# Kernel tuning notes

Hardware: AMD Instinct MI355X
Metric: run time of the kernel (lower is better)

Reference implementation:

```python
import jax, jax.numpy as jnp
import numpy as np

B, K, N, NBR = 4, 2048, 8192, 32
DIM, C_IN, W_HID, C_MID, F_HID, C_OUT = 3, 16, 32, 16, 64, 64
BIG = 3000.0


def _mlp(x, w1, b1, w2, b2):
    # SetTransform with one hidden layer, reduction='none': Linear->ReLU->Linear
    return jnp.maximum(x @ w1 + b1, 0.0) @ w2 + b2


def setup_inputs() -> dict:
    key = jax.random.key(0)
    ks = jax.random.split(key, 12)
    s = lambda fan_in: 1.0 / np.sqrt(fan_in)
    return {
        "keys": jax.random.normal(ks[0], (B, K, DIM), jnp.float32),
        "points": jax.random.normal(ks[1], (B, N, DIM), jnp.float32),
        "feats": jax.random.normal(ks[2], (B, N, C_IN), jnp.float32),
        "valid": jax.random.bernoulli(ks[3], 0.95, (B, K, N)),
        "ww1": jax.random.normal(ks[4], (DIM, W_HID), jnp.float32) * s(DIM),
        "wb1": jax.random.normal(ks[5], (W_HID,), jnp.float32) * s(DIM),
        "ww2": jax.random.normal(ks[6], (W_HID, C_MID), jnp.float32) * s(W_HID),
        "wb2": jax.random.normal(ks[7], (C_MID,), jnp.float32) * s(W_HID),
        "fw1": jax.random.normal(ks[8], (C_IN * C_MID, F_HID), jnp.float32) * s(C_IN * C_MID),
        "fb1": jax.random.normal(ks[9], (F_HID,), jnp.float32) * s(C_IN * C_MID),
        "fw2": jax.random.normal(ks[10], (F_HID, C_OUT), jnp.float32) * s(F_HID),
        "fb2": jax.random.normal(ks[11], (C_OUT,), jnp.float32) * s(F_HID),
    }


def reference(keys, points, feats, valid, ww1, wb1, ww2, wb2, fw1, fb1, fw2, fb2):
    # --- dist_fn (Euclidean): dist_vec = points - keys, dist = ||dist_vec|| ---
    diff = points[:, None, :, :] - keys[:, :, None, :]        # [B,K,N,DIM]
    dist = jnp.sqrt(jnp.sum(diff * diff, axis=-1))            # [B,K,N]
    big_dist = dist.max() * BIG
    dist = dist + jnp.where(valid, 0.0, big_dist)
    # --- kNN: smallest NBR distances per key ---
    _, idxs = jax.lax.top_k(-dist, NBR)                       # [B,K,NBR]
    bidx = jnp.arange(B)[:, None, None]
    # gather neighbor info (avoids materializing [B,K,N,*] gathered copies)
    n_rel = points[bidx, idxs] - keys[:, :, None, :]          # [B,K,NBR,DIM]
    n_feats = feats[bidx, idxs]                               # [B,K,NBR,C_IN]
    n_valid = jnp.take_along_axis(valid, idxs, axis=2)        # [B,K,NBR]
    n_valid = n_valid[..., None].astype(n_rel.dtype)
    # per-neighbor weight MLP, mask, batched matmul reduce over neighbors
    m = _mlp(n_rel, ww1, wb1, ww2, wb2) * n_valid             # [B,K,NBR,C_MID]
    nf = n_feats * n_valid                                    # [B,K,NBR,C_IN]
    e = jnp.einsum('bkqm,bkqc->bkmc', m, nf)                  # [B,K,C_MID,C_IN]
    e = e.reshape(B, K, C_MID * C_IN)
    return _mlp(e, fw1, fb1, fw2, fb2)                        # [B,K,C_OUT]
```

## Files before the change

kernel.cpp:

```cpp
#include <hip/hip_runtime.h>
#include <hip/hip_bf16.h>
#include <cstdint>
#include <cstddef>

#define B_    4
#define K_    2048
#define N_    8192
#define NBR_  32
#define NCAND 44
#define SELCAP 64
#define CIN   16
#define WHID  32
#define CMID  16
#define FHID  64
#define COUT  64
#define SOA_OFF 4096
#define WS_NEED ((size_t)SOA_OFF + (size_t)B_ * 3 * N_ * 4 + 4096 )

__global__ void pc_detect_kernel(const unsigned* __restrict__ v, int* __restrict__ flag) {
    const unsigned w = v[threadIdx.x & 63];
    const int byte_like = (((w & 0xFEFEFEFEu) == 0u) && ((w & 0xFFFFFF00u) != 0u)) ? 1 : 0;
    const unsigned long long m = __ballot(byte_like);
    if (threadIdx.x == 0) *flag = (m != 0ull) ? 1 : 0;
}

__global__ __launch_bounds__(256) void pc_soa_kernel(const float* __restrict__ pts,
                                                     float* __restrict__ soa) {
    const int i = blockIdx.x * 256 + threadIdx.x;
    const int b = i >> 13, n = i & (N_ - 1);
    const int t = n >> 8, w = n & 255;
    const float* p = pts + (size_t)i * 3;
    const float x = p[0], y = p[1], z = p[2];
    float* d = soa + (size_t)b * 3 * N_ + (size_t)t * 768 + w;
    d[0]   = x;
    d[256] = y;
    d[512] = z;
}

__device__ __forceinline__ unsigned umin_(unsigned a, unsigned b) { return a < b ? a : b; }

__device__ __forceinline__ unsigned med3_(unsigned a, unsigned b, unsigned c) {
    unsigned d;
    asm("v_med3_u32 %0, %1, %2, %3" : "=v"(d) : "v"(a), "v"(b), "v"(c));
    return d;
}
__device__ __forceinline__ void insert_m3(unsigned (&sa)[8], unsigned kv) {
#pragma unroll
    for (int i = 7; i >= 1; --i)
        sa[i] = med3_(sa[i - 1], sa[i], kv);
    sa[0] = umin_(sa[0], kv);
}

__device__ __forceinline__ void scan_tiled(const float* __restrict__ soa_b,
                                           float kx, float ky, float kz,
                                           int lane, unsigned (&sa)[8]) {
    const int voff = lane * 4;
    const float* p  = soa_b;
    float4 X = *(const float4*)(p + voff);
    float4 Y = *(const float4*)(p + 256 + voff);
    float4 Z = *(const float4*)(p + 512 + voff);
    unsigned vn = (unsigned)voff;
#pragma unroll 2
    for (int t = 0; t < 32; ++t) {
        const float4 cX = X, cY = Y, cZ = Z;
        const float* pn = p + 768;
        X = *(const float4*)(pn + voff);
        Y = *(const float4*)(pn + 256 + voff);
        Z = *(const float4*)(pn + 512 + voff);
        p = pn;
        float dx, dy, dz, d2;
#define PC_ONE(J, XX, YY, ZZ)                                                      \
        dx = XX - kx; dy = YY - ky; dz = ZZ - kz;                                  \
        d2 = fmaf(dz, dz, fmaf(dy, dy, dx * dx));                                  \
        insert_m3(sa, (__float_as_uint(d2) & 0xFFFFE000u) | (vn | J##u));
        PC_ONE(0, cX.x, cY.x, cZ.x)
        PC_ONE(1, cX.y, cY.y, cZ.y)
        PC_ONE(2, cX.z, cY.z, cZ.z)
        PC_ONE(3, cX.w, cY.w, cZ.w)
#undef PC_ONE
        vn += 256u;
    }
}

__device__ __forceinline__ void scan_aos4(const float* __restrict__ pts,
                                          float kx, float ky, float kz,
                                          int lane, unsigned (&sa)[8]) {
    const int l4 = lane * 4;
#pragma unroll 2
    for (int t = 0; t < N_ / 256; ++t) {
        const int n0 = t * 256 + l4;
        const float4* p4 = (const float4*)(pts + (size_t)n0 * 3);
        const float4 A = p4[0], Bv = p4[1], Cv = p4[2];
        float dx, dy, dz, d2;
        dx = A.x - kx; dy = A.y - ky; dz = A.z - kz;
        d2 = fmaf(dz, dz, fmaf(dy, dy, dx * dx));
        insert_m3(sa, (__float_as_uint(d2) & 0xFFFFE000u) | (unsigned)(n0 + 0));
        dx = A.w - kx; dy = Bv.x - ky; dz = Bv.y - kz;
        d2 = fmaf(dz, dz, fmaf(dy, dy, dx * dx));
        insert_m3(sa, (__float_as_uint(d2) & 0xFFFFE000u) | (unsigned)(n0 + 1));
        dx = Bv.z - kx; dy = Bv.w - ky; dz = Cv.x - kz;
        d2 = fmaf(dz, dz, fmaf(dy, dy, dx * dx));
        insert_m3(sa, (__float_as_uint(d2) & 0xFFFFE000u) | (unsigned)(n0 + 2));
        dx = Cv.y - kx; dy = Cv.z - ky; dz = Cv.w - kz;
        d2 = fmaf(dz, dz, fmaf(dy, dy, dx * dx));
        insert_m3(sa, (__float_as_uint(d2) & 0xFFFFE000u) | (unsigned)(n0 + 3));
    }
}

struct SelBuf {
    unsigned cnt;
    unsigned pad;
    unsigned key[SELCAP];
    unsigned long long fk[SELCAP];
};
struct Slice {
    union {
        SelBuf   sel;
        float    w[NBR_ * CMID];
        float    pad_[512];
    } A;
    union {
        float nf[NBR_ * CIN];
        struct { float hp[4 * FHID]; float hf[FHID]; } h;
    } Bv;
    union {
        unsigned slot[NBR_];
        float    e[CMID * CIN];
    } C;
};

template <int SOA>
__global__ __launch_bounds__(128, 8) void pc_main_kernel(
    const float* __restrict__ keys,
    const float* __restrict__ points,
    const float* __restrict__ soa,
    const float* __restrict__ feats,
    const void*  __restrict__ validp,
    const float* __restrict__ ww1, const float* __restrict__ wb1,
    const float* __restrict__ ww2, const float* __restrict__ wb2,
    const float* __restrict__ fw1, const float* __restrict__ fb1,
    const float* __restrict__ fw2, const float* __restrict__ fb2,
    float* __restrict__ out,
    const int* __restrict__ flagp)
{
    __shared__ Slice sl[2];

    const int lane = threadIdx.x & 63;
    const int wv   = threadIdx.x >> 6;
    const int row  = (blockIdx.x << 1) | wv;
    const int b    = row >> 11;
    Slice& S = sl[wv];

    const float kx = keys[row * 3 + 0];
    const float ky = keys[row * 3 + 1];
    const float kz = keys[row * 3 + 2];
    const float* pts = points + (size_t)b * N_ * 3;

    unsigned sa[8];
#pragma unroll
    for (int i = 0; i < 8; ++i) sa[i] = 0xFFFFFFFFu;

    if (SOA) scan_tiled(soa + (size_t)b * 3 * N_, kx, ky, kz, lane, sa);
    else     scan_aos4(pts, kx, ky, kz, lane, sa);

    unsigned hi[8];
#pragma unroll
    for (int s = 0; s < 8; ++s) hi[s] = sa[s] >> 13;

    unsigned want = 0u;
    int need = NCAND;
    for (int bb = 18; bb >= 0; --bb) {
        want <<= 1;
        int cnt0 = 0;
#pragma unroll
        for (int s = 0; s < 8; ++s)
            cnt0 += (int)__popcll(__ballot((hi[s] >> bb) == want));
        if (cnt0 < need) { need -= cnt0; want |= 1u; }
    }

    if (lane == 0) S.A.sel.cnt = 0u;
    int c = 0;
#pragma unroll
    for (int s = 0; s < 8; ++s) c += (hi[s] <= want) ? 1 : 0;
    unsigned base = 0u;
    if (c > 0) base = atomicAdd(&S.A.sel.cnt, (unsigned)c);
#pragma unroll
    for (int s = 0; s < 8; ++s)
        if (s < c && base + (unsigned)s < (unsigned)SELCAP)
            S.A.sel.key[base + s] = sa[s];
    unsigned stot = S.A.sel.cnt;
    stot = (unsigned)__builtin_amdgcn_readfirstlane((int)stot);
    if (stot > (unsigned)SELCAP) stot = SELCAP;
    asm volatile("" ::: "memory");

    if (lane < NBR_) S.C.slot[lane] = 0xFFFFFFFFu;

    const unsigned selkey = S.A.sel.key[(unsigned)lane < stot ? lane : 0];
    const int cidx = (int)(selkey & 8191u);
    unsigned vbit = 0u;
    unsigned long long fkey = ~0ull;
    if ((unsigned)lane < stot) {
        const float cdx = pts[cidx * 3 + 0] - kx;
        const float cdy = pts[cidx * 3 + 1] - ky;
        const float cdz = pts[cidx * 3 + 2] - kz;
        const float cd2 = fmaf(cdz, cdz, fmaf(cdy, cdy, cdx * cdx));
        const int flag = *flagp;
        const size_t vbase = (size_t)row * N_;
        if (flag) vbit = ((const unsigned char*)validp)[vbase + (size_t)cidx];
        else      vbit = ((const unsigned*)validp)[vbase + (size_t)cidx];
        const unsigned d2bits = (vbit != 0u) ? __float_as_uint(cd2) : 0xFFFFFFFFu;
        fkey = ((unsigned long long)d2bits << 13) | (unsigned long long)cidx;
        S.A.sel.fk[lane] = fkey;
    }
    asm volatile("" ::: "memory");

    {
        int rank = 0;
#pragma unroll 4
        for (unsigned j = 0; j < stot; ++j) {
            const unsigned long long fj = S.A.sel.fk[j];
            rank += (fj < fkey) ? 1 : 0;
        }
        if ((unsigned)lane < stot && vbit != 0u && rank < NBR_)
            S.C.slot[rank] = selkey;
    }
    asm volatile("" ::: "memory");

    const int q    = lane & 31;
    const int half = lane >> 5;
    const unsigned skey = S.C.slot[q];
    const int   nidx = (int)(skey & 8191u);
    const float vf   = (skey < 0xF0000000u) ? 1.0f : 0.0f;

    const float rx = pts[nidx * 3 + 0] - kx;
    const float ry = pts[nidx * 3 + 1] - ky;
    const float rz = pts[nidx * 3 + 2] - kz;
    asm volatile("" ::: "memory");

    float wacc[8];
    {
        const float4 b0 = *(const float4*)&wb2[half * 8 + 0];
        const float4 b1 = *(const float4*)&wb2[half * 8 + 4];
        wacc[0] = b0.x; wacc[1] = b0.y; wacc[2] = b0.z; wacc[3] = b0.w;
        wacc[4] = b1.x; wacc[5] = b1.y; wacc[6] = b1.z; wacc[7] = b1.w;
    }

#pragma unroll 8
    for (int j = 0; j < WHID; ++j) {
        float hj = fmaf(rx, ww1[j], fmaf(ry, ww1[WHID + j], fmaf(rz, ww1[2 * WHID + j], wb1[j])));
        hj = fmaxf(hj, 0.0f);
        const float4 wa = *(const float4*)&ww2[j * CMID + half * 8 + 0];
        const float4 wb = *(const float4*)&ww2[j * CMID + half * 8 + 4];
        wacc[0] = fmaf(hj, wa.x, wacc[0]);
        wacc[1] = fmaf(hj, wa.y, wacc[1]);
        wacc[2] = fmaf(hj, wa.z, wacc[2]);
        wacc[3] = fmaf(hj, wa.w, wacc[3]);
        wacc[4] = fmaf(hj, wb.x, wacc[4]);
        wacc[5] = fmaf(hj, wb.y, wacc[5]);
        wacc[6] = fmaf(hj, wb.z, wacc[6]);
        wacc[7] = fmaf(hj, wb.w, wacc[7]);
    }
#pragma unroll
    for (int m = 0; m < 8; ++m) wacc[m] *= vf;

    *(float4*)&S.A.w[q * CMID + half * 8 + 0] = make_float4(wacc[0], wacc[1], wacc[2], wacc[3]);
    *(float4*)&S.A.w[q * CMID + half * 8 + 4] = make_float4(wacc[4], wacc[5], wacc[6], wacc[7]);

    const float* fp = feats + ((size_t)b * N_ + (size_t)nidx) * CIN + half * 8;
    *(float4*)&S.Bv.nf[q * CIN + half * 8 + 0] = *(const float4*)(fp + 0);
    *(float4*)&S.Bv.nf[q * CIN + half * 8 + 4] = *(const float4*)(fp + 4);
    asm volatile("" ::: "memory");

    {
        const int m  = lane >> 2;
        const int c4 = lane & 3;
        float4 eacc = make_float4(0.f, 0.f, 0.f, 0.f);
#pragma unroll
        for (int qq = 0; qq < NBR_; ++qq) {
            const float  wq = S.A.w[qq * CMID + m];
            const float4 f  = *(const float4*)&S.Bv.nf[qq * CIN + c4 * 4];
            eacc.x = fmaf(wq, f.x, eacc.x);
            eacc.y = fmaf(wq, f.y, eacc.y);
            eacc.z = fmaf(wq, f.z, eacc.z);
            eacc.w = fmaf(wq, f.w, eacc.w);
        }
        *(float4*)&S.C.e[m * CIN + c4 * 4] = eacc;
    }
    asm volatile("" ::: "memory");

    {
        const int g  = lane >> 4;
        const int t4 = lane & 15;
        float a0 = 0.f, a1 = 0.f, a2 = 0.f, a3 = 0.f;
#pragma unroll 8
        for (int i = 0; i < 64; ++i) {
            const float  ev = S.C.e[g * 64 + i];
            const float4 wv2 = *(const float4*)&fw1[(size_t)(g * 64 + i) * FHID + t4 * 4];
            a0 = fmaf(ev, wv2.x, a0);
            a1 = fmaf(ev, wv2.y, a1);
            a2 = fmaf(ev, wv2.z, a2);
            a3 = fmaf(ev, wv2.w, a3);
        }
        *(float4*)&S.Bv.h.hp[g * FHID + t4 * 4] = make_float4(a0, a1, a2, a3);
    }
    asm volatile("" ::: "memory");

    {
        float hf = fb1[lane] + S.Bv.h.hp[lane] + S.Bv.h.hp[FHID + lane]
                 + S.Bv.h.hp[2 * FHID + lane] + S.Bv.h.hp[3 * FHID + lane];
        S.Bv.h.hf[lane] = fmaxf(hf, 0.0f);
    }
    asm volatile("" ::: "memory");

    {
        float oacc = fb2[lane];
#pragma unroll 8
        for (int j = 0; j < FHID; ++j)
            oacc = fmaf(S.Bv.h.hf[j], fw2[(size_t)j * COUT + lane], oacc);
        out[(size_t)row * COUT + lane] = oacc;
    }
}

extern "C" void kernel_launch(void* const* d_in, const int* in_sizes, int n_in,
                              void* d_out, int out_size, void* d_ws, size_t ws_size,
                              hipStream_t stream) {
    const float* keys   = (const float*)d_in[0];
    const float* points = (const float*)d_in[1];
    const float* feats  = (const float*)d_in[2];
    const void*  valid  = d_in[3];
    const float* ww1 = (const float*)d_in[4];
    const float* wb1 = (const float*)d_in[5];
    const float* ww2 = (const float*)d_in[6];
    const float* wb2 = (const float*)d_in[7];
    const float* fw1 = (const float*)d_in[8];
    const float* fb1 = (const float*)d_in[9];
    const float* fw2 = (const float*)d_in[10];
    const float* fb2 = (const float*)d_in[11];
    float* out = (float*)d_out;
    int*   flag = (int*)d_ws;
    float* soa  = (float*)((char*)d_ws + SOA_OFF);

    pc_detect_kernel<<<1, 64, 0, stream>>>((const unsigned*)valid, flag);

    if (ws_size >= WS_NEED) {
        pc_soa_kernel<<<(B_ * N_) / 256, 256, 0, stream>>>(points, soa);
        pc_main_kernel<1><<<(B_ * K_) / 2, 128, 0, stream>>>(
            keys, points, soa, feats, valid,
            ww1, wb1, ww2, wb2, fw1, fb1, fw2, fb2, out, flag);
    } else {
        pc_main_kernel<0><<<(B_ * K_) / 2, 128, 0, stream>>>(
            keys, points, soa, feats, valid,
            ww1, wb1, ww2, wb2, fw1, fb1, fw2, fb2, out, flag);
    }
}
```

Before: 394.9 us.

## Stage point tiles in shared memory shared across four waves per block

Blocks grow from two to four waves (one key row each), and the SoA point coordinates are cooperatively loaded into a double-buffered LDS tile, so the four waves share each global load instead of each wave streaming the whole point set from memory. A __syncthreads per tile adds barrier cost across 32 tiles, and LDS use rises with four slices per block, which can lower occupancy. The Slice storage is unioned with the staging buffer.

```diff
diff --git a/kernel.cpp b/kernel.cpp
--- a/kernel.cpp
+++ b/kernel.cpp
@@ -14,8 +14,10 @@
 #define CMID  16
 #define FHID  64
 #define COUT  64
+#define TILE_  256
+#define NTILES (N_ / TILE_)
 #define SOA_OFF 4096
-#define WS_NEED ((size_t)SOA_OFF + (size_t)B_ * 3 * N_ * 4 + 4096 )
+#define WS_NEED ((size_t)SOA_OFF + (size_t)B_ * 3 * N_ * 4 + 4096)
 
 __global__ void pc_detect_kernel(const unsigned* __restrict__ v, int* __restrict__ flag) {
     const unsigned w = v[threadIdx.x & 63];
@@ -49,37 +51,6 @@
     for (int i = 7; i >= 1; --i)
         sa[i] = med3_(sa[i - 1], sa[i], kv);
     sa[0] = umin_(sa[0], kv);
-}
-
-__device__ __forceinline__ void scan_tiled(const float* __restrict__ soa_b,
-                                           float kx, float ky, float kz,
-                                           int lane, unsigned (&sa)[8]) {
-    const int voff = lane * 4;
-    const float* p  = soa_b;
-    float4 X = *(const float4*)(p + voff);
-    float4 Y = *(const float4*)(p + 256 + voff);
-    float4 Z = *(const float4*)(p + 512 + voff);
-    unsigned vn = (unsigned)voff;
-#pragma unroll 2
-    for (int t = 0; t < 32; ++t) {
-        const float4 cX = X, cY = Y, cZ = Z;
-        const float* pn = p + 768;
-        X = *(const float4*)(pn + voff);
-        Y = *(const float4*)(pn + 256 + voff);
-        Z = *(const float4*)(pn + 512 + voff);
-        p = pn;
-        float dx, dy, dz, d2;
-#define PC_ONE(J, XX, YY, ZZ)                                                      \
-        dx = XX - kx; dy = YY - ky; dz = ZZ - kz;                                  \
-        d2 = fmaf(dz, dz, fmaf(dy, dy, dx * dx));                                  \
-        insert_m3(sa, (__float_as_uint(d2) & 0xFFFFE000u) | (vn | J##u));
-        PC_ONE(0, cX.x, cY.x, cZ.x)
-        PC_ONE(1, cX.y, cY.y, cZ.y)
-        PC_ONE(2, cX.z, cY.z, cZ.z)
-        PC_ONE(3, cX.w, cY.w, cZ.w)
-#undef PC_ONE
-        vn += 256u;
-    }
 }
 
 __device__ __forceinline__ void scan_aos4(const float* __restrict__ pts,
@@ -128,9 +99,13 @@
         float    e[CMID * CIN];
     } C;
 };
+union BlockMem {
+    float stage[2][768];
+    Slice sl[4];
+};
 
 template <int SOA>
-__global__ __launch_bounds__(128, 8) void pc_main_kernel(
+__global__ __launch_bounds__(256, 8) void pc_main_kernel(
     const float* __restrict__ keys,
     const float* __restrict__ points,
     const float* __restrict__ soa,
@@ -143,13 +118,14 @@
     float* __restrict__ out,
     const int* __restrict__ flagp)
 {
-    __shared__ Slice sl[2];
-
-    const int lane = threadIdx.x & 63;
-    const int wv   = threadIdx.x >> 6;
-    const int row  = (blockIdx.x << 1) | wv;
+    __shared__ BlockMem bm;
+
+    const int tid  = threadIdx.x;
+    const int lane = tid & 63;
+    const int wv   = tid >> 6;
+    const int row  = (blockIdx.x << 2) | wv;
     const int b    = row >> 11;
-    Slice& S = sl[wv];
+    Slice& S = bm.sl[wv];
 
     const float kx = keys[row * 3 + 0];
     const float ky = keys[row * 3 + 1];
@@ -160,8 +136,39 @@
 #pragma unroll
     for (int i = 0; i < 8; ++i) sa[i] = 0xFFFFFFFFu;
 
-    if (SOA) scan_tiled(soa + (size_t)b * 3 * N_, kx, ky, kz, lane, sa);
-    else     scan_aos4(pts, kx, ky, kz, lane, sa);
+    if (SOA) {
+        const float* sb = soa + (size_t)b * 3 * N_;
+        if (tid < 192)
+            *(float4*)&bm.stage[0][tid * 4] = *(const float4*)(sb + tid * 4);
+        __syncthreads();
+        for (int t = 0; t < NTILES; ++t) {
+            float4 nx;
+            const bool do_stage = (t + 1 < NTILES) && (tid < 192);
+            if (do_stage)
+                nx = *(const float4*)(sb + (size_t)(t + 1) * 768 + tid * 4);
+            const float* cur = bm.stage[t & 1];
+            const float4 X = *(const float4*)(cur + lane * 4);
+            const float4 Y = *(const float4*)(cur + 256 + lane * 4);
+            const float4 Z = *(const float4*)(cur + 512 + lane * 4);
+            const unsigned vn = (unsigned)(t * 256 + lane * 4);
+            float dx, dy, dz, d2;
+#define PC_ONE(J, XX, YY, ZZ)                                                      \
+            dx = XX - kx; dy = YY - ky; dz = ZZ - kz;                              \
+            d2 = fmaf(dz, dz, fmaf(dy, dy, dx * dx));                              \
+            insert_m3(sa, (__float_as_uint(d2) & 0xFFFFE000u) | (vn | J##u));
+            PC_ONE(0, X.x, Y.x, Z.x)
+            PC_ONE(1, X.y, Y.y, Z.y)
+            PC_ONE(2, X.z, Y.z, Z.z)
+            PC_ONE(3, X.w, Y.w, Z.w)
+#undef PC_ONE
+            if (do_stage)
+                *(float4*)&bm.stage[(t + 1) & 1][tid * 4] = nx;
+            __syncthreads();
+        }
+    } else {
+        scan_aos4(pts, kx, ky, kz, lane, sa);
+        __syncthreads();
+    }
 
     unsigned hi[8];
 #pragma unroll
@@ -344,11 +351,11 @@
 
     if (ws_size >= WS_NEED) {
         pc_soa_kernel<<<(B_ * N_) / 256, 256, 0, stream>>>(points, soa);
-        pc_main_kernel<1><<<(B_ * K_) / 2, 128, 0, stream>>>(
+        pc_main_kernel<1><<<(B_ * K_) / 4, 256, 0, stream>>>(
             keys, points, soa, feats, valid,
             ww1, wb1, ww2, wb2, fw1, fb1, fw2, fb2, out, flag);
     } else {
-        pc_main_kernel<0><<<(B_ * K_) / 2, 128, 0, stream>>>(
+        pc_main_kernel<0><<<(B_ * K_) / 4, 256, 0, stream>>>(
             keys, points, soa, feats, valid,
             ww1, wb1, ww2, wb2, fw1, fb1, fw2, fb2, out, flag);
     }
```

Result: no change. 400.7 us (+1.5%).
